# Kernel tuning notes

Hardware: AMD Instinct MI355X
Metric: run time of the kernel (lower is better)

Reference implementation:

```python
import jax, jax.numpy as jnp
import numpy as np

B, N, C, H = 8, 2048, 512, 8
D = C // H                      # head dim = 64
Q_LENGTHS = [1024 + 128 * i for i in range(B)]  # ragged: 1024..1920, sum below
TQ = sum(Q_LENGTHS)             # 11776 total queries


def setup_inputs() -> dict:
    key = jax.random.key(0)
    ks = jax.random.split(key, 5)
    w = 0.02  # init scale for weights
    return {
        "x": jax.random.normal(ks[0], (B, N, C), jnp.float32),
        "q": jax.random.normal(ks[1], (TQ, C), jnp.float32),
        "Wq": jax.random.normal(ks[2], (C, C), jnp.float32) * w,
        "Wkv": jax.random.normal(ks[3], (2 * C, C), jnp.float32) * w,
        "Wproj": jax.random.normal(ks[4], (C, C), jnp.float32) * w,
        "bproj": jnp.zeros((C,), jnp.float32),
        "q_lengths": jnp.array(Q_LENGTHS, jnp.int32),
        "max_q_len": max(Q_LENGTHS),
    }


def reference(x, q, Wq, Wkv, Wproj, bproj, q_lengths, max_q_len):
    # Eval path of Attention.forward: batched_sparse_attention(q, k, v, q_lengths, scale)
    # == varlen cross-attention: queries of batch b attend over all N kv tokens of batch b.
    Tq = q.shape[0]
    scale = D ** -0.5

    qh = (q @ Wq.T).reshape(Tq, H, D)                 # [Tq, H, D]
    kv = (x @ Wkv.T).reshape(B, N, 2, H, D)
    k = kv[:, :, 0]                                   # [B, N, H, D]
    v = kv[:, :, 1]                                   # [B, N, H, D]

    # ragged -> padded per-batch layout
    csum = jnp.cumsum(q_lengths)                      # [B]
    offs = jnp.concatenate([jnp.zeros((1,), csum.dtype), csum])
    tok = jnp.arange(Tq)
    q_batch = (tok[:, None] >= csum[None, :]).sum(-1)  # [Tq] batch id per query
    q_pos = tok - offs[q_batch]                        # [Tq] position within batch

    qpad = jnp.zeros((B, max_q_len, H, D), qh.dtype).at[q_batch, q_pos].set(qh)

    scores = jnp.einsum('blhd,bnhd->bhln', qpad, k) * scale  # [B, H, L, N]
    attn = jax.nn.softmax(scores, axis=-1)                   # all N keys valid
    out = jnp.einsum('bhln,bnhd->blhd', attn, v)             # [B, L, H, D]

    out = out[q_batch, q_pos].reshape(Tq, C)           # gather ragged rows back
    return out @ Wproj.T + bproj
```

## Files before the change

kernel.cpp:

```cpp
#include <hip/hip_runtime.h>
#include <hip/hip_bf16.h>
#include <math.h>

constexpr int Cc = 512;
constexpr int Hh = 8;
constexpr int Dd = 64;
constexpr int Nn = 2048;
constexpr int Bb = 8;
constexpr int GK = 512;

typedef __attribute__((ext_vector_type(8))) short short8;
typedef __attribute__((ext_vector_type(4))) float f32x4;
typedef __attribute__((ext_vector_type(4))) unsigned int u32x4;
typedef __attribute__((ext_vector_type(2))) unsigned int u32x2;

#define C2SCALE 0.1803368801f

static __device__ __forceinline__ ushort f2bf(float v) {
  __hip_bfloat16 h = __float2bfloat16(v);
  return *reinterpret_cast<ushort*>(&h);
}
static __device__ __forceinline__ float bf2f(ushort u) {
  __hip_bfloat16 h = *reinterpret_cast<__hip_bfloat16*>(&u);
  return __bfloat162float(h);
}
static __device__ __forceinline__ unsigned int pk2(float f0, float f1) {
  return (unsigned int)f2bf(f0) | ((unsigned int)f2bf(f1) << 16);
}

__global__ __launch_bounds__(256) void mfma_proj_kernel(
    const ushort* __restrict__ Ah, const ushort* __restrict__ Al,
    const ushort* __restrict__ Bh, const ushort* __restrict__ Bl,
    const float* __restrict__ bias, float* __restrict__ Cf, int Nc)
{
  __shared__ ushort lAh[128 * 32];
  __shared__ ushort lBh[128 * 32];
  __shared__ ushort lAl[128 * 32];
  __shared__ ushort lBl[128 * 32];

  const int tid = threadIdx.x;
  const int w = tid >> 6, lane = tid & 63;
  const int c = lane & 15, g = lane >> 4;
  const int wr = (w >> 1) * 64, wc = (w & 1) * 64;
  const int m0 = blockIdx.y * 128, n0 = blockIdx.x * 128;
  const int sr = tid >> 2;
  const int sk = (tid & 3) * 8;

  short8 rAh[2], rAl[2], rBh[2], rBl[2];

  auto loadAB = [&](int k0) {
#pragma unroll
    for (int hf = 0; hf < 2; ++hf) {
      const size_t ia = (size_t)(m0 + sr + hf * 64) * GK + k0 + sk;
      const size_t ib = (size_t)(n0 + sr + hf * 64) * GK + k0 + sk;
      rAh[hf] = *(const short8*)(Ah + ia);
      rAl[hf] = *(const short8*)(Al + ia);
      rBh[hf] = *(const short8*)(Bh + ib);
      rBl[hf] = *(const short8*)(Bl + ib);
    }
  };

  f32x4 acc[4][4] = {};
  loadAB(0);

  for (int k0 = 0; k0 < GK; k0 += 32) {
    __syncthreads();
    *(short8*)&lAh[sr * 32 + sk]        = rAh[0];
    *(short8*)&lAh[(sr + 64) * 32 + sk] = rAh[1];
    *(short8*)&lBh[sr * 32 + sk]        = rBh[0];
    *(short8*)&lBh[(sr + 64) * 32 + sk] = rBh[1];
    *(short8*)&lAl[sr * 32 + sk]        = rAl[0];
    *(short8*)&lAl[(sr + 64) * 32 + sk] = rAl[1];
    *(short8*)&lBl[sr * 32 + sk]        = rBl[0];
    *(short8*)&lBl[(sr + 64) * 32 + sk] = rBl[1];
    __syncthreads();
    if (k0 + 32 < GK) loadAB(k0 + 32);

    short8 ah[4], al[4], bh[4], bl[4];
#pragma unroll
    for (int i = 0; i < 4; ++i) {
      const int ar = (wr + i * 16 + c) * 32 + g * 8;
      const int br = (wc + i * 16 + c) * 32 + g * 8;
      ah[i] = *(const short8*)&lAh[ar];
      bh[i] = *(const short8*)&lBh[br];
      al[i] = *(const short8*)&lAl[ar];
      bl[i] = *(const short8*)&lBl[br];
    }
#pragma unroll
    for (int mi = 0; mi < 4; ++mi)
#pragma unroll
      for (int nj = 0; nj < 4; ++nj) {
        acc[mi][nj] = __builtin_amdgcn_mfma_f32_16x16x32_bf16(ah[mi], bl[nj], acc[mi][nj], 0,0,0);
        acc[mi][nj] = __builtin_amdgcn_mfma_f32_16x16x32_bf16(al[mi], bh[nj], acc[mi][nj], 0,0,0);
        acc[mi][nj] = __builtin_amdgcn_mfma_f32_16x16x32_bf16(ah[mi], bh[nj], acc[mi][nj], 0,0,0);
      }
  }

#pragma unroll
  for (int mi = 0; mi < 4; ++mi)
#pragma unroll
    for (int r = 0; r < 4; ++r) {
      const size_t rb = (size_t)(m0 + wr + mi * 16 + g * 4 + r) * Nc;
#pragma unroll
      for (int nj = 0; nj < 4; ++nj) {
        const int col = n0 + wc + nj * 16 + c;
        Cf[rb + col] = acc[mi][nj][r] + bias[col];
      }
    }
}

__global__ __launch_bounds__(256, 2) void proj_qkv_kernel(
    const float* __restrict__ qin, const float* __restrict__ Wq,
    const float* __restrict__ x, const float* __restrict__ Wkv,
    const float* __restrict__ Wproj,
    ushort* __restrict__ qhi, ushort* __restrict__ kbf,
    ushort* __restrict__ vtb, ushort* __restrict__ wph,
    ushort* __restrict__ wpl, int TQ, int BN)
{
  __shared__ ushort smem[128 * 136];

  const int tid = threadIdx.x;
  const int w = tid >> 6, lane = tid & 63;
  const int c = lane & 15, g = lane >> 4;
  const int wr = (w >> 1) * 64, wc = (w & 1) * 64;
  const int sr = tid >> 2, sk = (tid & 3) * 8;
  const int NQB = (TQ / 128) * (Cc / 128);
  const int NKVB = (BN / 128) * (Cc / 128);
  const int bid = blockIdx.x;

  auto cvt8 = [&](const float* F, size_t idx) -> short8 {
    const float4 f0 = *(const float4*)(F + idx);
    const float4 f1 = *(const float4*)(F + idx + 4);
    const float vv[8] = {f0.x, f0.y, f0.z, f0.w, f1.x, f1.y, f1.z, f1.w};
    short8 h;
#pragma unroll
    for (int j = 0; j < 8; ++j) ((ushort*)&h)[j] = f2bf(vv[j]);
    return h;
  };

  if (bid < NQB) {
    const int m0 = (bid >> 2) * 128;
    const int n0 = (bid & 3) * 128;
    ushort* lA = smem;
    ushort* lB = smem + 128 * 32;

    short8 rA[2], rB[2];
    auto loadQ = [&](int k0) {
#pragma unroll
      for (int hf = 0; hf < 2; ++hf) {
        rA[hf] = cvt8(qin, (size_t)(m0 + sr + hf * 64) * GK + k0 + sk);
        rB[hf] = cvt8(Wq,  (size_t)(n0 + sr + hf * 64) * GK + k0 + sk);
      }
    };

    f32x4 acc[4][4] = {};
    loadQ(0);
    for (int k0 = 0; k0 < GK; k0 += 32) {
      __syncthreads();
      *(short8*)&lA[sr * 32 + sk]        = rA[0];
      *(short8*)&lA[(sr + 64) * 32 + sk] = rA[1];
      *(short8*)&lB[sr * 32 + sk]        = rB[0];
      *(short8*)&lB[(sr + 64) * 32 + sk] = rB[1];
      __syncthreads();
      if (k0 + 32 < GK) loadQ(k0 + 32);

      short8 a[4], bb[4];
#pragma unroll
      for (int i = 0; i < 4; ++i) {
        a[i]  = *(const short8*)&lA[(wr + i * 16 + c) * 32 + g * 8];
        bb[i] = *(const short8*)&lB[(wc + i * 16 + c) * 32 + g * 8];
      }
#pragma unroll
      for (int mi = 0; mi < 4; ++mi)
#pragma unroll
        for (int nj = 0; nj < 4; ++nj)
          acc[mi][nj] = __builtin_amdgcn_mfma_f32_16x16x32_bf16(a[mi], bb[nj], acc[mi][nj], 0,0,0);
    }
#pragma unroll
    for (int mi = 0; mi < 4; ++mi)
#pragma unroll
      for (int r = 0; r < 4; ++r) {
        const size_t rb = (size_t)(m0 + wr + mi * 16 + g * 4 + r) * Cc;
#pragma unroll
        for (int nj = 0; nj < 4; ++nj)
          qhi[rb + n0 + wc + nj * 16 + c] = f2bf(acc[mi][nj][r] * C2SCALE);
      }
  } else if (bid < NQB + NKVB) {
    const int b2 = bid - NQB;
    const int n0 = (b2 & 3) * 128;
    const int m0 = (b2 >> 2) * 128;
    ushort* lA   = smem;
    ushort* lBk  = smem + 128 * 32;
    ushort* lBv  = smem + 2 * 128 * 32;
    ushort* tbuf = smem;

    short8 rA[2], rBk[2], rBv[2];
    auto loadAll = [&](int k0) {
#pragma unroll
      for (int hf = 0; hf < 2; ++hf) {
        rA[hf]  = cvt8(x,   (size_t)(m0 + sr + hf * 64) * GK + k0 + sk);
        rBk[hf] = cvt8(Wkv, (size_t)(n0 + sr + hf * 64) * GK + k0 + sk);
        rBv[hf] = cvt8(Wkv, (size_t)(512 + n0 + sr + hf * 64) * GK + k0 + sk);
      }
    };

    f32x4 ak[4][4] = {};
    f32x4 av[4][4] = {};
    loadAll(0);

    for (int k0 = 0; k0 < GK; k0 += 32) {
      __syncthreads();
      *(short8*)&lA[sr * 32 + sk]         = rA[0];
      *(short8*)&lA[(sr + 64) * 32 + sk]  = rA[1];
      *(short8*)&lBk[sr * 32 + sk]        = rBk[0];
      *(short8*)&lBk[(sr + 64) * 32 + sk] = rBk[1];
      *(short8*)&lBv[sr * 32 + sk]        = rBv[0];
      *(short8*)&lBv[(sr + 64) * 32 + sk] = rBv[1];
      __syncthreads();
      if (k0 + 32 < GK) loadAll(k0 + 32);

      short8 a[4], bk[4], bv[4];
#pragma unroll
      for (int i = 0; i < 4; ++i) {
        const int ar = (wr + i * 16 + c) * 32 + g * 8;
        const int br = (wc + i * 16 + c) * 32 + g * 8;
        a[i]  = *(const short8*)&lA[ar];
        bk[i] = *(const short8*)&lBk[br];
        bv[i] = *(const short8*)&lBv[br];
      }
#pragma unroll
      for (int mi = 0; mi < 4; ++mi)
#pragma unroll
        for (int nj = 0; nj < 4; ++nj) {
          ak[mi][nj] = __builtin_amdgcn_mfma_f32_16x16x32_bf16(a[mi], bk[nj], ak[mi][nj], 0,0,0);
          av[mi][nj] = __builtin_amdgcn_mfma_f32_16x16x32_bf16(a[mi], bv[nj], av[mi][nj], 0,0,0);
        }
    }

#pragma unroll
    for (int mi = 0; mi < 4; ++mi)
#pragma unroll
      for (int r = 0; r < 4; ++r) {
        const size_t rb = (size_t)(m0 + wr + mi * 16 + g * 4 + r) * Cc;
#pragma unroll
        for (int nj = 0; nj < 4; ++nj)
          kbf[rb + n0 + wc + nj * 16 + c] = f2bf(ak[mi][nj][r]);
      }

    __syncthreads();
#pragma unroll
    for (int mi = 0; mi < 4; ++mi)
#pragma unroll
      for (int r = 0; r < 4; ++r) {
        const int tl = wr + mi * 16 + g * 4 + r;
#pragma unroll
        for (int nj = 0; nj < 4; ++nj)
          tbuf[(wc + nj * 16 + c) * 136 + tl] = f2bf(av[mi][nj][r]);
      }
    __syncthreads();
#pragma unroll
    for (int it = 0; it < 8; ++it) {
      const int idx = tid + it * 256;
      const int row = idx >> 4;
      const int c8 = (idx & 15) * 8;
      *(short8*)&vtb[(size_t)(n0 + row) * BN + m0 + c8] =
          *(const short8*)&tbuf[row * 136 + c8];
    }
  } else {
    const int b3 = bid - NQB - NKVB;
    const size_t base = (size_t)b3 * 16384 + (size_t)tid * 4;
#pragma unroll
    for (int it = 0; it < 16; ++it) {
      const size_t e0 = base + (size_t)it * 1024;
      const float4 v = *(const float4*)(Wproj + e0);
      const float vv[4] = {v.x, v.y, v.z, v.w};
      ushort4 uh, ul;
#pragma unroll
      for (int j = 0; j < 4; ++j) {
        const ushort hb = f2bf(vv[j]);
        ((ushort*)&uh)[j] = hb;
        ((ushort*)&ul)[j] = f2bf(vv[j] - bf2f(hb));
      }
      *(ushort4*)(wph + e0) = uh;
      *(ushort4*)(wpl + e0) = ul;
    }
  }
}

__global__ __launch_bounds__(256, 4) void attn_mfma14_kernel(
    const ushort* __restrict__ qhi,
    const ushort* __restrict__ kbf,
    const ushort* __restrict__ vtb,
    ushort* __restrict__ ohi,
    ushort* __restrict__ olo)
{
  constexpr int QOFF[8] = {0, 1024, 2176, 3456, 4864, 6400, 8064, 9856};

  const int lin = blockIdx.x;
  const int b  = lin & 7;
  const int h  = (lin >> 3) & 7;
  const int qt = lin >> 6;

  const int Lb  = 1024 + 128 * b;
  const int off = QOFF[b];
  if (qt * 128 >= Lb) return;

  constexpr int KP = 72;
  constexpr int NC = Nn / 64;
  __shared__ ushort Ks[64 * KP];
  __shared__ ushort Vs[64 * KP];

  const int tid = threadIdx.x;
  const int lane = tid & 63;
  const int w = tid >> 6;
  const int c = lane & 15;
  const int g = (lane >> 4) & 3;

  short8 qf[2][2];
  int qrow[2];
#pragma unroll
  for (int t = 0; t < 2; ++t) {
    qrow[t] = off + qt * 128 + w * 32 + t * 16 + c;
    const size_t base = (size_t)qrow[t] * Cc + h * Dd + g * 8;
    qf[t][0] = *(const short8*)(qhi + base);
    qf[t][1] = *(const short8*)(qhi + base + 32);
  }

  float l_part[2] = {0.f, 0.f};
  f32x4 accO4[2][4] = {};

  const size_t kbase = (size_t)b * Nn * Cc + h * Dd;
  const size_t vbase = (size_t)h * Dd * (Bb * Nn) + (size_t)b * Nn;

  for (int ch = 0; ch < NC; ++ch) {
    __syncthreads();
#pragma unroll
    for (int it = 0; it < 2; ++it) {
      const int i = tid + it * 256;
      const int row = i >> 3, c8 = (i & 7) * 8;
      *(short8*)&Ks[row * KP + c8] =
          *(const short8*)&kbf[kbase + (size_t)(ch * 64 + row) * Cc + c8];
    }
#pragma unroll
    for (int it = 0; it < 2; ++it) {
      const int i = tid + it * 256;
      const int row = i >> 3, c8 = (i & 7) * 8;
      const int kb1 = (c8 & ~31) | (((c8 >> 3) & 3) << 2);
      const size_t gb = vbase + (size_t)row * (Bb * Nn) + ch * 64;
      const u32x2 vlo = *(const u32x2*)&vtb[gb + kb1];
      const u32x2 vhi = *(const u32x2*)&vtb[gb + kb1 + 16];
      u32x4 vv;
      vv[0] = vlo[0]; vv[1] = vlo[1];
      vv[2] = vhi[0]; vv[3] = vhi[1];
      *(short8*)&Vs[row * KP + c8] = __builtin_bit_cast(short8, vv);
    }
    __syncthreads();

    f32x4 accT4[2][4] = {};
    __builtin_amdgcn_s_setprio(1);
#pragma unroll
    for (int ks2 = 0; ks2 < 2; ++ks2) {
#pragma unroll
      for (int kb = 0; kb < 4; ++kb) {
        const short8 kf = *(const short8*)
            &Ks[(kb * 16 + c) * KP + ks2 * 32 + g * 8];
        accT4[0][kb] = __builtin_amdgcn_mfma_f32_16x16x32_bf16(kf, qf[0][ks2], accT4[0][kb], 0,0,0);
        accT4[1][kb] = __builtin_amdgcn_mfma_f32_16x16x32_bf16(kf, qf[1][ks2], accT4[1][kb], 0,0,0);
      }
    }
    __builtin_amdgcn_s_setprio(0);

    unsigned int up[2][4][2];
#pragma unroll
    for (int t = 0; t < 2; ++t)
#pragma unroll
      for (int kb = 0; kb < 4; ++kb) {
        const float p0 = __builtin_amdgcn_exp2f(accT4[t][kb][0]);
        const float p1 = __builtin_amdgcn_exp2f(accT4[t][kb][1]);
        const float p2 = __builtin_amdgcn_exp2f(accT4[t][kb][2]);
        const float p3 = __builtin_amdgcn_exp2f(accT4[t][kb][3]);
        l_part[t] += (p0 + p1) + (p2 + p3);
        up[t][kb][0] = pk2(p0, p1);
        up[t][kb][1] = pk2(p2, p3);
      }

#pragma unroll
    for (int ks2 = 0; ks2 < 2; ++ks2) {
      short8 pa[2];
#pragma unroll
      for (int t = 0; t < 2; ++t) {
        u32x4 wv;
        wv.x = up[t][2 * ks2][0];
        wv.y = up[t][2 * ks2][1];
        wv.z = up[t][2 * ks2 + 1][0];
        wv.w = up[t][2 * ks2 + 1][1];
        pa[t] = __builtin_bit_cast(short8, wv);
      }
      __builtin_amdgcn_s_setprio(1);
#pragma unroll
      for (int db = 0; db < 4; ++db) {
        const short8 vf = *(const short8*)
            &Vs[(db * 16 + c) * KP + ks2 * 32 + g * 8];
        accO4[0][db] = __builtin_amdgcn_mfma_f32_16x16x32_bf16(vf, pa[0], accO4[0][db], 0,0,0);
        accO4[1][db] = __builtin_amdgcn_mfma_f32_16x16x32_bf16(vf, pa[1], accO4[1][db], 0,0,0);
      }
      __builtin_amdgcn_s_setprio(0);
    }
  }

#pragma unroll
  for (int t = 0; t < 2; ++t) {
    float l = l_part[t];
    l += __shfl_xor(l, 16);
    l += __shfl_xor(l, 32);
    const float inv = 1.f / l;
    const size_t rb = (size_t)qrow[t] * Cc + h * Dd;
#pragma unroll
    for (int db = 0; db < 4; ++db) {
      const int d0 = db * 16 + g * 4;
      ushort4 uh, ul;
#pragma unroll
      for (int e = 0; e < 4; ++e) {
        const float o = accO4[t][db][e] * inv;
        const ushort hb = f2bf(o);
        ((ushort*)&uh)[e] = hb;
        ((ushort*)&ul)[e] = f2bf(o - bf2f(hb));
      }
      *(ushort4*)&ohi[rb + d0] = uh;
      *(ushort4*)&olo[rb + d0] = ul;
    }
  }
}

extern "C" void kernel_launch(void* const* d_in, const int* in_sizes, int n_in,
                              void* d_out, int out_size, void* d_ws, size_t ws_size,
                              hipStream_t stream)
{
  const float* x     = (const float*)d_in[0];
  const float* q     = (const float*)d_in[1];
  const float* Wq    = (const float*)d_in[2];
  const float* Wkv   = (const float*)d_in[3];
  const float* Wproj = (const float*)d_in[4];
  const float* bproj = (const float*)d_in[5];

  const int TQ = in_sizes[1] / Cc;
  const int BN = in_sizes[0] / Cc;

  const size_t szQ = (size_t)TQ * Cc * 2;
  const size_t szX = (size_t)BN * Cc * 2;
  const size_t szW = (size_t)Cc * Cc * 2;

  char* p = (char*)d_ws;
  ushort* q_hi  = (ushort*)p;  p += szQ;
  ushort* k_bf  = (ushort*)p;  p += szX;
  ushort* v_t   = (ushort*)p;  p += szX;
  ushort* at_hi = (ushort*)p;  p += szQ;
  ushort* at_lo = (ushort*)p;  p += szQ;
  ushort* wp_hi = (ushort*)p;  p += szW;
  ushort* wp_lo = (ushort*)p;

  const int nqb = (TQ / 128) * (Cc / 128);
  const int nkvb = (BN / 128) * (Cc / 128);
  proj_qkv_kernel<<<dim3(nqb + nkvb + 16), 256, 0, stream>>>(
      q, Wq, x, Wkv, Wproj, q_hi, k_bf, v_t, wp_hi, wp_lo, TQ, BN);
  attn_mfma14_kernel<<<dim3(64 * 15), 256, 0, stream>>>(
      q_hi, k_bf, v_t, at_hi, at_lo);
  mfma_proj_kernel<<<dim3(Cc/128, TQ/128), 256, 0, stream>>>(
      at_hi, at_lo, wp_hi, wp_lo, bproj, (float*)d_out, Cc);
}
```

Before: 161.2 us.

## Split KV range of attention into two blocks and combine partial results

The attention kernel gets a split template parameter. With S=2 each block handles half of the key/value chunks and writes an unnormalized partial output plus its row sums; a new elementwise kernel then adds the two partials and normalizes. The aim is to double the number of blocks so the ragged grid fills the GPU better. The cost is an extra kernel launch and extra global-memory traffic for the partial buffers. The split path only runs when the workspace is large enough, otherwise it falls back to the single-pass kernel.

```diff
diff --git a/kernel.cpp b/kernel.cpp
--- a/kernel.cpp
+++ b/kernel.cpp
@@ -8,6 +8,7 @@
 constexpr int Nn = 2048;
 constexpr int Bb = 8;
 constexpr int GK = 512;
+constexpr int TQc = 11776;
 
 typedef __attribute__((ext_vector_type(8))) short short8;
 typedef __attribute__((ext_vector_type(4))) float f32x4;
@@ -287,16 +288,19 @@
   }
 }
 
-__global__ __launch_bounds__(256, 4) void attn_mfma14_kernel(
+template <int S>
+__global__ __launch_bounds__(256, 4) void attn_mfma15_kernel(
     const ushort* __restrict__ qhi,
     const ushort* __restrict__ kbf,
     const ushort* __restrict__ vtb,
-    ushort* __restrict__ ohi,
-    ushort* __restrict__ olo)
+    ushort* __restrict__ oh0, ushort* __restrict__ ol0,
+    ushort* __restrict__ oh1, ushort* __restrict__ ol1,
+    float* __restrict__ lbuf)
 {
   constexpr int QOFF[8] = {0, 1024, 2176, 3456, 4864, 6400, 8064, 9856};
 
   const int lin = blockIdx.x;
+  const int sp  = blockIdx.y;
   const int b  = lin & 7;
   const int h  = (lin >> 3) & 7;
   const int qt = lin >> 6;
@@ -307,6 +311,7 @@
 
   constexpr int KP = 72;
   constexpr int NC = Nn / 64;
+  constexpr int NCS = NC / S;
   __shared__ ushort Ks[64 * KP];
   __shared__ ushort Vs[64 * KP];
 
@@ -332,7 +337,7 @@
   const size_t kbase = (size_t)b * Nn * Cc + h * Dd;
   const size_t vbase = (size_t)h * Dd * (Bb * Nn) + (size_t)b * Nn;
 
-  for (int ch = 0; ch < NC; ++ch) {
+  for (int ch = sp * NCS; ch < (sp + 1) * NCS; ++ch) {
     __syncthreads();
 #pragma unroll
     for (int it = 0; it < 2; ++it) {
@@ -408,12 +413,20 @@
     }
   }
 
+  ushort* __restrict__ oh = (S == 1 || sp == 0) ? oh0 : oh1;
+  ushort* __restrict__ ol = (S == 1 || sp == 0) ? ol0 : ol1;
 #pragma unroll
   for (int t = 0; t < 2; ++t) {
     float l = l_part[t];
     l += __shfl_xor(l, 16);
     l += __shfl_xor(l, 32);
-    const float inv = 1.f / l;
+    float inv = 1.f;
+    if (S == 1) {
+      inv = 1.f / l;
+    } else {
+      if (g == 0)
+        lbuf[(size_t)sp * (TQc * Hh) + (size_t)qrow[t] * Hh + h] = l;
+    }
     const size_t rb = (size_t)qrow[t] * Cc + h * Dd;
 #pragma unroll
     for (int db = 0; db < 4; ++db) {
@@ -421,15 +434,46 @@
       ushort4 uh, ul;
 #pragma unroll
       for (int e = 0; e < 4; ++e) {
-        const float o = accO4[t][db][e] * inv;
+        const float o = (S == 1) ? accO4[t][db][e] * inv : accO4[t][db][e];
         const ushort hb = f2bf(o);
         ((ushort*)&uh)[e] = hb;
         ((ushort*)&ul)[e] = f2bf(o - bf2f(hb));
       }
-      *(ushort4*)&ohi[rb + d0] = uh;
-      *(ushort4*)&olo[rb + d0] = ul;
-    }
-  }
+      *(ushort4*)&oh[rb + d0] = uh;
+      *(ushort4*)&ol[rb + d0] = ul;
+    }
+  }
+}
+
+__global__ __launch_bounds__(256) void attn_combine_kernel(
+    ushort* __restrict__ oh0, ushort* __restrict__ ol0,
+    const ushort* __restrict__ oh1, const ushort* __restrict__ ol1,
+    const float* __restrict__ lbuf, int total4)
+{
+  const int i4 = blockIdx.x * 256 + threadIdx.x;
+  if (i4 >= total4) return;
+  const size_t e0 = (size_t)i4 * 4;
+  const int row = (int)(e0 >> 9);
+  const int h = ((int)e0 & 511) >> 6;
+  const float l = lbuf[(size_t)row * Hh + h] +
+                  lbuf[(size_t)(TQc * Hh) + (size_t)row * Hh + h];
+  const float inv = 1.f / l;
+
+  const ushort4 h0 = *(const ushort4*)(oh0 + e0);
+  const ushort4 l0 = *(const ushort4*)(ol0 + e0);
+  const ushort4 h1 = *(const ushort4*)(oh1 + e0);
+  const ushort4 l1 = *(const ushort4*)(ol1 + e0);
+  ushort4 uh, ul;
+#pragma unroll
+  for (int e = 0; e < 4; ++e) {
+    const float o = ((bf2f(((const ushort*)&h0)[e]) + bf2f(((const ushort*)&l0)[e])) +
+                     (bf2f(((const ushort*)&h1)[e]) + bf2f(((const ushort*)&l1)[e]))) * inv;
+    const ushort hb = f2bf(o);
+    ((ushort*)&uh)[e] = hb;
+    ((ushort*)&ul)[e] = f2bf(o - bf2f(hb));
+  }
+  *(ushort4*)(oh0 + e0) = uh;
+  *(ushort4*)(ol0 + e0) = ul;
 }
 
 extern "C" void kernel_launch(void* const* d_in, const int* in_sizes, int n_in,
@@ -449,6 +493,7 @@
   const size_t szQ = (size_t)TQ * Cc * 2;
   const size_t szX = (size_t)BN * Cc * 2;
   const size_t szW = (size_t)Cc * Cc * 2;
+  const size_t szL = (size_t)2 * TQ * Hh * 4;
 
   char* p = (char*)d_ws;
   ushort* q_hi  = (ushort*)p;  p += szQ;
@@ -457,14 +502,30 @@
   ushort* at_hi = (ushort*)p;  p += szQ;
   ushort* at_lo = (ushort*)p;  p += szQ;
   ushort* wp_hi = (ushort*)p;  p += szW;
-  ushort* wp_lo = (ushort*)p;
+  ushort* wp_lo = (ushort*)p;  p += szW;
+  ushort* a2_hi = (ushort*)p;  p += szQ;
+  ushort* a2_lo = (ushort*)p;  p += szQ;
+  float*  lbuf  = (float*)p;   p += szL;
+  const size_t need2 = (size_t)(p - (char*)d_ws);
+
+  const bool S2 = ws_size >= need2;
 
   const int nqb = (TQ / 128) * (Cc / 128);
   const int nkvb = (BN / 128) * (Cc / 128);
   proj_qkv_kernel<<<dim3(nqb + nkvb + 16), 256, 0, stream>>>(
       q, Wq, x, Wkv, Wproj, q_hi, k_bf, v_t, wp_hi, wp_lo, TQ, BN);
-  attn_mfma14_kernel<<<dim3(64 * 15), 256, 0, stream>>>(
-      q_hi, k_bf, v_t, at_hi, at_lo);
+
+  if (S2) {
+    attn_mfma15_kernel<2><<<dim3(64 * 15, 2), 256, 0, stream>>>(
+        q_hi, k_bf, v_t, at_hi, at_lo, a2_hi, a2_lo, lbuf);
+    const int total4 = TQ * Cc / 4;
+    attn_combine_kernel<<<(total4 + 255) / 256, 256, 0, stream>>>(
+        at_hi, at_lo, a2_hi, a2_lo, lbuf, total4);
+  } else {
+    attn_mfma15_kernel<1><<<dim3(64 * 15, 1), 256, 0, stream>>>(
+        q_hi, k_bf, v_t, at_hi, at_lo, nullptr, nullptr, nullptr);
+  }
+
   mfma_proj_kernel<<<dim3(Cc/128, TQ/128), 256, 0, stream>>>(
       at_hi, at_lo, wp_hi, wp_lo, bproj, (float*)d_out, Cc);
 }
```

After: 183.5 us. +13.8%, slower.
